# Kernel optimization log

Measured on AMD Instinct MI355X. Metric: run time of the kernel, lower is better.

## Reference

```python
import jax, jax.numpy as jnp
import numpy as np

B, S, D, H = 8, 1024, 1024, 16
HD = D // H  # 64


def setup_inputs() -> dict:
    key = jax.random.key(0)
    ks = jax.random.split(key, 10)
    f32 = jnp.float32
    inp = {
        "query": jax.random.normal(ks[0], (B, S, D), f32),
        "key": jax.random.normal(ks[1], (B, S, D), f32),
        "value": jax.random.normal(ks[2], (B, S, D), f32),
        "rel": jax.random.normal(ks[3], (B, S, S), f32),
        "timestamp": jax.random.normal(ks[4], (B, S, S), f32),
        "mask": jax.random.randint(ks[5], (B, S, S), 0, 2).astype(bool),
        "l1": jnp.float32(0.3),
        "l2": jnp.float32(0.5),
        "encode_pos": 0,
        "Wq": jax.random.normal(ks[6], (D, D), f32) * 0.02,
        "bq": jnp.zeros((D,), f32),
        "Wk": jax.random.normal(ks[7], (D, D), f32) * 0.02,
        "bk": jnp.zeros((D,), f32),
        "Wv": jax.random.normal(ks[8], (D, D), f32) * 0.02,
        "bv": jnp.zeros((D,), f32),
    }
    return inp


def _proj(x, W, b):
    # nn.Linear: x @ W.T + b, then split heads -> [B, H, S, HD]
    y = x @ W.T + b
    return y.reshape(B, S, H, HD).transpose(0, 2, 1, 3)


def reference(query, key, value, rel, timestamp, mask, l1, l2, encode_pos,
              Wq, bq, Wk, bk, Wv, bv):
    # encode_pos == 0 path: QK^T + time-decay + rel-attn three-softmax blend
    q = _proj(query, Wq, bq)
    k = _proj(key, Wk, bk)
    v = _proj(value, Wv, bv)

    m = mask[:, None]                       # [B,1,S,S], broadcasts over heads
    mf = m.astype(jnp.float32)

    # rel attention: zero out where mask is False, then fill zeros with -1e5
    rel_m = rel[:, None] * mf               # [B,1,S,S]
    rel_attn = jax.nn.softmax(jnp.where(rel_m == 0, -100000.0, rel_m), axis=-1)

    inv_sqrt_d = 1.0 / np.sqrt(HD).astype(np.float32)
    scores = jnp.einsum("bhqd,bhkd->bhqk", q, k) * inv_sqrt_d
    scores = jnp.where(m, -1e32, scores)

    time_stamp = jnp.exp(-jnp.abs(timestamp[:, None]))   # [B,1,S,S]
    time_stamp = jnp.where(m, -100000.0, time_stamp)

    prob_attn = jax.nn.softmax(scores, axis=-1)          # [B,H,S,S]
    time_attn = jax.nn.softmax(time_stamp, axis=-1)      # [B,1,S,S]

    prob_attn = (1.0 - l2) * prob_attn + l2 * time_attn
    prob_attn = (1.0 - l1) * prob_attn + l1 * rel_attn
    # dropout is identity at inference

    out = jnp.einsum("bhqk,bhkd->bhqd", prob_attn, v)
    out = out.transpose(0, 2, 1, 3).reshape(B, S, D)
    return out, prob_attn
```

## Files before the change

kernel.cpp:

```cpp
#include <hip/hip_runtime.h>
#include <stdint.h>

typedef short bf16x8 __attribute__((ext_vector_type(8)));
typedef short bf16x4 __attribute__((ext_vector_type(4)));
typedef float f32x4 __attribute__((ext_vector_type(4)));
typedef unsigned short u16x4 __attribute__((ext_vector_type(4)));
typedef unsigned short u16x8 __attribute__((ext_vector_type(8)));

constexpr int NB = 8, NS = 1024, ND = 1024, NH = 16, NHD = 64;

static __device__ __forceinline__ unsigned short f2bf(float f) {
    union { float f; uint32_t u; } v; v.f = f;
    uint32_t r = (v.u + 0x7fffu + ((v.u >> 16) & 1u)) >> 16;
    return (unsigned short)r;
}

static __device__ __forceinline__ f32x4 mfma32(bf16x8 a, bf16x8 b, f32x4 c) {
    return __builtin_amdgcn_mfma_f32_16x16x32_bf16(a, b, c, 0, 0, 0);
}

static __device__ __forceinline__ f32x4 mfma16(bf16x4 a, bf16x4 b, f32x4 c) {
#if __has_builtin(__builtin_amdgcn_mfma_f32_16x16x16bf16_1k)
    return __builtin_amdgcn_mfma_f32_16x16x16bf16_1k(a, b, c, 0, 0, 0);
#elif __has_builtin(__builtin_amdgcn_mfma_f32_16x16x16_bf16)
    return __builtin_amdgcn_mfma_f32_16x16x16_bf16(a, b, c, 0, 0, 0);
#else
    asm volatile("v_mfma_f32_16x16x16_bf16 %0, %1, %2, %0\n\ts_nop 7\n\ts_nop 7"
                 : "+v"(c) : "v"(a), "v"(b));
    return c;
#endif
}

static __device__ __forceinline__ bool mask_at(const void* m, size_t idx, int ms) {
    if (ms == 4) return ((const unsigned int*)m)[idx] != 0u;
    return ((const unsigned char*)m)[idx] != 0;
}

__global__ void detect_mask(const unsigned int* __restrict__ m, int* __restrict__ flag) {
    int l = threadIdx.x;
    bool bad = false;
    for (int i = l; i < 1024; i += 64) {
        unsigned int w = m[i];
        bad |= (w > 1u && w != 0x3f800000u);
    }
    bad = (bool)__any(bad);
    if (l == 0) *flag = bad ? 1 : 4;
}

__global__ __launch_bounds__(256) void cvt_frag(const float* __restrict__ in,
                                                unsigned short* __restrict__ out, int n8) {
    int stride = gridDim.x * blockDim.x;
    for (int idx = blockIdx.x * blockDim.x + threadIdx.x; idx < n8; idx += stride) {
        const float4* p = (const float4*)in + 2 * (size_t)idx;
        float4 a = p[0], b = p[1];
        u16x8 o;
        o[0] = f2bf(a.x); o[1] = f2bf(a.y); o[2] = f2bf(a.z); o[3] = f2bf(a.w);
        o[4] = f2bf(b.x); o[5] = f2bf(b.y); o[6] = f2bf(b.z); o[7] = f2bf(b.w);
        int m = idx >> 7, c8 = idx & 127;
        int kt = c8 >> 2, sub = c8 & 3;
        int lane = (m & 15) + 16 * sub;
        size_t slot = ((size_t)(m >> 4) * 32 + kt) * 64 + lane;
        *(u16x8*)(out + slot * 8) = o;
    }
}

__global__ __launch_bounds__(256) void proj_gemm(const unsigned short* __restrict__ Af,
                                                 const unsigned short* __restrict__ Wf,
                                                 const float* __restrict__ bias,
                                                 unsigned short* __restrict__ C, int mode) {
    int l = threadIdx.x & 63, w = threadIdx.x >> 6;
    int lr = l & 15, lg = l >> 4;
    int m_base = blockIdx.x * 128 + (w >> 1) * 64;
    int n_base = blockIdx.y * 128 + (w & 1) * 64;
    int mtg0 = m_base >> 4, ntg0 = n_base >> 4;
    f32x4 acc[4][4] = {};
    for (int kt = 0; kt < 32; kt++) {
        bf16x8 af[4], bfr[4];
        #pragma unroll
        for (int mt = 0; mt < 4; mt++)
            af[mt] = *(const bf16x8*)(Af + (((size_t)(mtg0 + mt) * 32 + kt) * 64 + l) * 8);
        #pragma unroll
        for (int nt = 0; nt < 4; nt++)
            bfr[nt] = *(const bf16x8*)(Wf + (((size_t)(ntg0 + nt) * 32 + kt) * 64 + l) * 8);
        #pragma unroll
        for (int mt = 0; mt < 4; mt++) {
            #pragma unroll
            for (int nt = 0; nt < 4; nt++)
                acc[mt][nt] = mfma32(af[mt], bfr[nt], acc[mt][nt]);
        }
    }
    #pragma unroll
    for (int mt = 0; mt < 4; mt++) {
        #pragma unroll
        for (int nt = 0; nt < 4; nt++) {
            int col = n_base + nt * 16 + lr;
            int row0 = m_base + mt * 16 + lg * 4;
            float bv = bias[col];
            int b = row0 >> 10;
            int h = col >> 6;
            if (mode == 0) {
                int st = (row0 & 1023) >> 4;
                int d32 = (col & 63) >> 5;
                int sub = (col & 31) >> 3;
                int e = col & 7;
                size_t base = ((((size_t)(b * NH + h) * 64 + st) * 2 + d32) * 64) * 8;
                #pragma unroll
                for (int r = 0; r < 4; r++) {
                    int lane = lg * 4 + r + 16 * sub;
                    C[base + (size_t)lane * 8 + e] = f2bf(acc[mt][nt][r] + bv);
                }
            } else {
                int s0 = row0 & 1023;
                int tg = s0 >> 4;
                int wv = tg >> 4;
                int t_in = tg & 15;
                int tp = t_in >> 1, half = t_in & 1;
                int dd = col & 63;
                int dt = dd >> 4;
                int lane = (dd & 15) + 16 * lg;
                u16x4 pk;
                #pragma unroll
                for (int r = 0; r < 4; r++) pk[r] = f2bf(acc[mt][nt][r] + bv);
                size_t addr = (((((size_t)(b * NH + h) * 4 + wv) * 8 + tp) * 4 + dt) * 64 + lane) * 8
                              + half * 4;
                *(u16x4*)(C + addr) = pk;
            }
        }
    }
}

__global__ __launch_bounds__(256) void tr_kernel(const float* __restrict__ rel,
                                                 const float* __restrict__ ts,
                                                 const void* __restrict__ maskp,
                                                 const int* __restrict__ msflag,
                                                 const float* __restrict__ l1p,
                                                 const float* __restrict__ l2p,
                                                 float* __restrict__ TRf,
                                                 uint32_t* __restrict__ PMf) {
    __shared__ float s_tm[4], s_rm[4], s_ts[4], s_rs[4];
    __shared__ unsigned char s_nib[256];
    int row = blockIdx.x;
    int t = threadIdx.x, w = t >> 6, l = t & 63;
    int ms = *msflag;
    size_t base = (size_t)row * NS;
    float4 r4 = ((const float4*)(rel + base))[t];
    float4 t4 = ((const float4*)(ts + base))[t];
    float rr[4], tt[4];
    *(float4*)rr = r4; *(float4*)tt = t4;
    float tv[4], rv[4];
    unsigned nib = 0;
    float tmx = -3.0e38f, rmx = -3.0e38f;
    #pragma unroll
    for (int j = 0; j < 4; j++) {
        bool m = mask_at(maskp, base + t * 4 + j, ms);
        nib |= (m ? 1u : 0u) << j;
        tv[j] = m ? -100000.0f : __expf(-fabsf(tt[j]));
        float rm_ = m ? rr[j] : 0.0f;
        rv[j] = (rm_ == 0.0f) ? -100000.0f : rm_;
        tmx = fmaxf(tmx, tv[j]); rmx = fmaxf(rmx, rv[j]);
    }
    s_nib[t] = (unsigned char)nib;
    #pragma unroll
    for (int off = 1; off < 64; off <<= 1) {
        tmx = fmaxf(tmx, __shfl_xor(tmx, off));
        rmx = fmaxf(rmx, __shfl_xor(rmx, off));
    }
    if (l == 0) { s_tm[w] = tmx; s_rm[w] = rmx; }
    __syncthreads();
    tmx = fmaxf(fmaxf(s_tm[0], s_tm[1]), fmaxf(s_tm[2], s_tm[3]));
    rmx = fmaxf(fmaxf(s_rm[0], s_rm[1]), fmaxf(s_rm[2], s_rm[3]));
    float te[4], re[4], tsum = 0.f, rsum = 0.f;
    #pragma unroll
    for (int j = 0; j < 4; j++) {
        te[j] = __expf(tv[j] - tmx); tsum += te[j];
        re[j] = __expf(rv[j] - rmx); rsum += re[j];
    }
    #pragma unroll
    for (int off = 1; off < 64; off <<= 1) {
        tsum += __shfl_xor(tsum, off);
        rsum += __shfl_xor(rsum, off);
    }
    if (l == 0) { s_ts[w] = tsum; s_rs[w] = rsum; }
    __syncthreads();
    tsum = s_ts[0] + s_ts[1] + s_ts[2] + s_ts[3];
    rsum = s_rs[0] + s_rs[1] + s_rs[2] + s_rs[3];
    float l1 = *l1p, l2 = *l2p;
    float ti = ((1.0f - l1) * l2) / tsum;
    float ri = l1 / rsum;
    float4 o;
    o.x = te[0] * ti + re[0] * ri;
    o.y = te[1] * ti + re[1] * ri;
    o.z = te[2] * ti + re[2] * ri;
    o.w = te[3] * ti + re[3] * ri;
    int b = row >> 10, q = row & 1023;
    int qt = q >> 4, qr = q & 15;
    size_t slot = ((((size_t)(b * 64 + qt) * 4 + (t >> 6)) * 16 + ((t >> 2) & 15)) * 64
                   + (qr + 16 * (t & 3)));
    ((float4*)TRf)[slot] = o;
    if (t < 32) {
        uint32_t word = 0;
        #pragma unroll
        for (int i = 0; i < 8; i++)
            word |= ((uint32_t)s_nib[t * 8 + i]) << (i * 4);
        PMf[(((size_t)(b * 64 + qt) * 4 + (t >> 3)) * 16 + qr) * 8 + (t & 7)] = word;
    }
}

__global__ __launch_bounds__(256) void att_pv_kernel(const unsigned short* __restrict__ Qf,
                                                     const unsigned short* __restrict__ Kf,
                                                     const uint32_t* __restrict__ PMf,
                                                     const float* __restrict__ TRf,
                                                     const float* __restrict__ l1p,
                                                     const float* __restrict__ l2p,
                                                     const unsigned short* __restrict__ Vf,
                                                     float* __restrict__ probOut,
                                                     float* __restrict__ outp) {
    __shared__ float reds[4][16];
    __shared__ f32x4 pacc[4][4][64];
    int bid = blockIdx.x;
    int swz = ((bid & 7) << 10) | (bid >> 3);
    int qt = swz & 63;
    int h = (swz >> 6) & 15;
    int b = swz >> 10;
    int tid = threadIdx.x, w = tid >> 6, l = tid & 63, lr = l & 15, lg = l >> 4;
    int q0 = qt * 16;
    int k_base = w * 256;
    int q = q0 + lr;
    size_t bh = (size_t)(b * NH + h);

    const unsigned short* qf = Qf + (((bh * 64 + qt) * 2) * 64 + l) * 8;
    bf16x8 bq0 = *(const bf16x8*)(qf);
    bf16x8 bq1 = *(const bf16x8*)(qf + 64 * 8);

    const uint32_t* pmp = PMf + (((size_t)(b * 64 + qt) * 4 + w) * 16 + lr) * 8;
    uint32_t pm[8];
    *(uint4*)(pm) = *(const uint4*)(pmp);
    *(uint4*)(pm + 4) = *(const uint4*)(pmp + 4);

    f32x4 acc[16] = {};
    const unsigned short* kfb = Kf + (((bh * 64 + w * 16) * 2) * 64) * 8 + (size_t)l * 8;
    #pragma unroll
    for (int t = 0; t < 16; t++) {
        const unsigned short* kp = kfb + (size_t)t * 2 * 64 * 8;
        bf16x8 a0 = *(const bf16x8*)(kp);
        bf16x8 a1 = *(const bf16x8*)(kp + 64 * 8);
        acc[t] = mfma32(a0, bq0, acc[t]);
        acc[t] = mfma32(a1, bq1, acc[t]);
    }
    float sm = 0.f;
    #pragma unroll
    for (int t = 0; t < 16; t++) {
        uint32_t word = pm[t >> 1];
        int shift = (t & 1) * 16 + lg * 4;
        #pragma unroll
        for (int r = 0; r < 4; r++) {
            bool m = (word >> (shift + r)) & 1u;
            float e = m ? 0.0f : __expf(acc[t][r] * 0.125f);
            acc[t][r] = e;
            sm += e;
        }
    }
    sm += __shfl_xor(sm, 16);
    sm += __shfl_xor(sm, 32);
    if (l < 16) reds[w][l] = sm;
    __syncthreads();
    float total = reds[0][lr] + reds[1][lr] + reds[2][lr] + reds[3][lr];
    float l1 = *l1p, l2 = *l2p;
    float rinv = ((1.0f - l1) * (1.0f - l2)) / total;

    float* po = probOut + bh * NS * NS + (size_t)q * NS + k_base;
    const float* trf = TRf + ((((size_t)(b * 64 + qt) * 4 + w) * 16) * 64 + l) * 4;
    const unsigned short* vf = Vf + ((((size_t)bh * 4 + w) * 8 * 4) * 64 + (size_t)l) * 8;
    f32x4 acc2[4] = {};
    #pragma unroll
    for (int tp = 0; tp < 8; tp++) {
        bf16x4 pfa, pfb;
        #pragma unroll
        for (int hf = 0; hf < 2; hf++) {
            int t = tp * 2 + hf;
            float4 tr4 = *(const float4*)(trf + t * 256);
            float4 o;
            o.x = acc[t][0] * rinv + tr4.x;
            o.y = acc[t][1] * rinv + tr4.y;
            o.z = acc[t][2] * rinv + tr4.z;
            o.w = acc[t][3] * rinv + tr4.w;
            *(float4*)(po + t * 16 + lg * 4) = o;
            bf16x4 pk;
            pk[0] = (short)f2bf(o.x); pk[1] = (short)f2bf(o.y);
            pk[2] = (short)f2bf(o.z); pk[3] = (short)f2bf(o.w);
            if (hf == 0) pfa = pk; else pfb = pk;
        }
        #pragma unroll
        for (int dt = 0; dt < 4; dt++) {
            bf16x8 vv = *(const bf16x8*)(vf + (size_t)(tp * 4 + dt) * 64 * 8);
            bf16x4 v0 = __builtin_shufflevector(vv, vv, 0, 1, 2, 3);
            bf16x4 v1 = __builtin_shufflevector(vv, vv, 4, 5, 6, 7);
            acc2[dt] = mfma16(v0, pfa, acc2[dt]);
            acc2[dt] = mfma16(v1, pfb, acc2[dt]);
        }
    }
    #pragma unroll
    for (int dt = 0; dt < 4; dt++) pacc[w][dt][l] = acc2[dt];
    __syncthreads();
    f32x4 s4 = pacc[0][w][l] + pacc[1][w][l] + pacc[2][w][l] + pacc[3][w][l];
    float4 ov;
    ov.x = s4[0]; ov.y = s4[1]; ov.z = s4[2]; ov.w = s4[3];
    *(float4*)(outp + ((size_t)b * NS + q0 + lr) * ND + h * NHD + w * 16 + lg * 4) = ov;
}

extern "C" void kernel_launch(void* const* d_in, const int* in_sizes, int n_in,
                              void* d_out, int out_size, void* d_ws, size_t ws_size,
                              hipStream_t stream) {
    const float* query = (const float*)d_in[0];
    const float* key   = (const float*)d_in[1];
    const float* value = (const float*)d_in[2];
    const float* rel   = (const float*)d_in[3];
    const float* ts    = (const float*)d_in[4];
    const void*  mask  = d_in[5];
    const float* l1p   = (const float*)d_in[6];
    const float* l2p   = (const float*)d_in[7];
    const float* Wq = (const float*)d_in[9];
    const float* bq = (const float*)d_in[10];
    const float* Wk = (const float*)d_in[11];
    const float* bk = (const float*)d_in[12];
    const float* Wv = (const float*)d_in[13];
    const float* bv = (const float*)d_in[14];

    char* ws = (char*)d_ws;
    const size_t SZ = (size_t)NB * NS * ND * 2;
    unsigned short* Qf  = (unsigned short*)(ws);
    unsigned short* Kf  = (unsigned short*)(ws + SZ);
    unsigned short* Vf  = (unsigned short*)(ws + 2 * SZ);
    unsigned short* Afq = (unsigned short*)(ws + 3 * SZ);
    unsigned short* Afk = (unsigned short*)(ws + 4 * SZ);
    unsigned short* Afv = (unsigned short*)(ws + 5 * SZ);
    unsigned short* Wfq = (unsigned short*)(ws + 6 * SZ);
    unsigned short* Wfk = (unsigned short*)(ws + 6 * SZ + 2u * 1024 * 1024);
    unsigned short* Wfv = (unsigned short*)(ws + 6 * SZ + 4u * 1024 * 1024);
    int* msflag         = (int*)(ws + 6 * SZ + 6u * 1024 * 1024);
    uint32_t* PMf       = (uint32_t*)(ws + 6 * SZ + 8u * 1024 * 1024);
    float* TRf = (float*)(ws + 3 * SZ);

    detect_mask<<<1, 64, 0, stream>>>((const unsigned int*)mask, msflag);

    const int nX8 = NB * NS * ND / 8;
    const int nW8 = 1024 * 1024 / 8;
    cvt_frag<<<1024, 256, 0, stream>>>(query, Afq, nX8);
    cvt_frag<<<1024, 256, 0, stream>>>(key,   Afk, nX8);
    cvt_frag<<<1024, 256, 0, stream>>>(value, Afv, nX8);
    cvt_frag<<<256, 256, 0, stream>>>(Wq, Wfq, nW8);
    cvt_frag<<<256, 256, 0, stream>>>(Wk, Wfk, nW8);
    cvt_frag<<<256, 256, 0, stream>>>(Wv, Wfv, nW8);

    dim3 pg(64, 8);
    proj_gemm<<<pg, 256, 0, stream>>>(Afq, Wfq, bq, Qf, 0);
    proj_gemm<<<pg, 256, 0, stream>>>(Afk, Wfk, bk, Kf, 0);
    proj_gemm<<<pg, 256, 0, stream>>>(Afv, Wfv, bv, Vf, 1);

    tr_kernel<<<NB * NS, 256, 0, stream>>>(rel, ts, mask, msflag, l1p, l2p, TRf, PMf);

    float* outp = (float*)d_out;
    float* probOut = outp + (size_t)NB * NS * ND;
    att_pv_kernel<<<NB * NH * (NS / 16), 256, 0, stream>>>(Qf, Kf, PMf, TRf, l1p, l2p, Vf,
                                                           probOut, outp);
}
```

Measured before the change: 572.8 us.

## Use single-wave attention blocks that recompute QK^T instead of splitting keys

Each attention block now uses one 64-thread wave covering all 1024 keys for a 16-query tile, instead of four waves each covering 256 keys. The cross-wave LDS reductions and __syncthreads for the softmax denominator and PV partials are gone. QK^T is computed twice, once for the row sum and again when writing probabilities, so the 16 score accumulators no longer have to stay in registers. V, TR and mask layouts are rearranged to match the per-wave key ordering. The cost is doubled QK MFMA work and K reads, plus longer serial work per wave.

```diff
diff --git a/kernel.cpp b/kernel.cpp
--- a/kernel.cpp
+++ b/kernel.cpp
@@ -112,16 +112,14 @@
             } else {
                 int s0 = row0 & 1023;
                 int tg = s0 >> 4;
-                int wv = tg >> 4;
-                int t_in = tg & 15;
-                int tp = t_in >> 1, half = t_in & 1;
+                int tp = tg >> 1, half = tg & 1;
                 int dd = col & 63;
                 int dt = dd >> 4;
                 int lane = (dd & 15) + 16 * lg;
                 u16x4 pk;
                 #pragma unroll
                 for (int r = 0; r < 4; r++) pk[r] = f2bf(acc[mt][nt][r] + bv);
-                size_t addr = (((((size_t)(b * NH + h) * 4 + wv) * 8 + tp) * 4 + dt) * 64 + lane) * 8
+                size_t addr = ((((size_t)(b * NH + h) * 32 + tp) * 4 + dt) * 64 + lane) * 8
                               + half * 4;
                 *(u16x4*)(C + addr) = pk;
             }
@@ -194,37 +192,33 @@
     o.w = te[3] * ti + re[3] * ri;
     int b = row >> 10, q = row & 1023;
     int qt = q >> 4, qr = q & 15;
-    size_t slot = ((((size_t)(b * 64 + qt) * 4 + (t >> 6)) * 16 + ((t >> 2) & 15)) * 64
-                   + (qr + 16 * (t & 3)));
+    size_t slot = ((size_t)(b * 64 + qt) * 64 + (t >> 2)) * 64 + (qr + 16 * (t & 3));
     ((float4*)TRf)[slot] = o;
     if (t < 32) {
         uint32_t word = 0;
         #pragma unroll
         for (int i = 0; i < 8; i++)
             word |= ((uint32_t)s_nib[t * 8 + i]) << (i * 4);
-        PMf[(((size_t)(b * 64 + qt) * 4 + (t >> 3)) * 16 + qr) * 8 + (t & 7)] = word;
-    }
-}
-
-__global__ __launch_bounds__(256) void att_pv_kernel(const unsigned short* __restrict__ Qf,
-                                                     const unsigned short* __restrict__ Kf,
-                                                     const uint32_t* __restrict__ PMf,
-                                                     const float* __restrict__ TRf,
-                                                     const float* __restrict__ l1p,
-                                                     const float* __restrict__ l2p,
-                                                     const unsigned short* __restrict__ Vf,
-                                                     float* __restrict__ probOut,
-                                                     float* __restrict__ outp) {
-    __shared__ float reds[4][16];
-    __shared__ f32x4 pacc[4][4][64];
+        PMf[((size_t)(b * 64 + qt) * 16 + qr) * 32 + t] = word;
+    }
+}
+
+__global__ __launch_bounds__(64, 4) void att_pv_kernel(const unsigned short* __restrict__ Qf,
+                                                       const unsigned short* __restrict__ Kf,
+                                                       const uint32_t* __restrict__ PMf,
+                                                       const float* __restrict__ TRf,
+                                                       const float* __restrict__ l1p,
+                                                       const float* __restrict__ l2p,
+                                                       const unsigned short* __restrict__ Vf,
+                                                       float* __restrict__ probOut,
+                                                       float* __restrict__ outp) {
     int bid = blockIdx.x;
     int swz = ((bid & 7) << 10) | (bid >> 3);
     int qt = swz & 63;
     int h = (swz >> 6) & 15;
     int b = swz >> 10;
-    int tid = threadIdx.x, w = tid >> 6, l = tid & 63, lr = l & 15, lg = l >> 4;
+    int l = threadIdx.x, lr = l & 15, lg = l >> 4;
     int q0 = qt * 16;
-    int k_base = w * 256;
     int q = q0 + lr;
     size_t bh = (size_t)(b * NH + h);
 
@@ -232,80 +226,91 @@
     bf16x8 bq0 = *(const bf16x8*)(qf);
     bf16x8 bq1 = *(const bf16x8*)(qf + 64 * 8);
 
-    const uint32_t* pmp = PMf + (((size_t)(b * 64 + qt) * 4 + w) * 16 + lr) * 8;
-    uint32_t pm[8];
-    *(uint4*)(pm) = *(const uint4*)(pmp);
-    *(uint4*)(pm + 4) = *(const uint4*)(pmp + 4);
-
-    f32x4 acc[16] = {};
-    const unsigned short* kfb = Kf + (((bh * 64 + w * 16) * 2) * 64) * 8 + (size_t)l * 8;
-    #pragma unroll
-    for (int t = 0; t < 16; t++) {
-        const unsigned short* kp = kfb + (size_t)t * 2 * 64 * 8;
-        bf16x8 a0 = *(const bf16x8*)(kp);
-        bf16x8 a1 = *(const bf16x8*)(kp + 64 * 8);
-        acc[t] = mfma32(a0, bq0, acc[t]);
-        acc[t] = mfma32(a1, bq1, acc[t]);
-    }
+    const unsigned short* kfb = Kf + ((bh * 64 * 2) * 64) * 8 + (size_t)l * 8;
+    const uint32_t* pmrow = PMf + ((size_t)(b * 64 + qt) * 16 + lr) * 32;
+
     float sm = 0.f;
-    #pragma unroll
-    for (int t = 0; t < 16; t++) {
-        uint32_t word = pm[t >> 1];
-        int shift = (t & 1) * 16 + lg * 4;
-        #pragma unroll
-        for (int r = 0; r < 4; r++) {
-            bool m = (word >> (shift + r)) & 1u;
-            float e = m ? 0.0f : __expf(acc[t][r] * 0.125f);
-            acc[t][r] = e;
-            sm += e;
+    for (int t8 = 0; t8 < 8; t8++) {
+        uint32_t pmw[4];
+        *(uint4*)pmw = *(const uint4*)(pmrow + t8 * 4);
+        #pragma unroll
+        for (int tt = 0; tt < 8; tt++) {
+            int t = t8 * 8 + tt;
+            const unsigned short* kp = kfb + (size_t)t * 1024;
+            bf16x8 a0 = *(const bf16x8*)kp;
+            bf16x8 a1 = *(const bf16x8*)(kp + 512);
+            f32x4 acc = {};
+            acc = mfma32(a0, bq0, acc);
+            acc = mfma32(a1, bq1, acc);
+            uint32_t word = pmw[tt >> 1];
+            int shift = (tt & 1) * 16 + lg * 4;
+            #pragma unroll
+            for (int r = 0; r < 4; r++) {
+                bool m = (word >> (shift + r)) & 1u;
+                sm += m ? 0.0f : __expf(acc[r] * 0.125f);
+            }
         }
     }
     sm += __shfl_xor(sm, 16);
     sm += __shfl_xor(sm, 32);
-    if (l < 16) reds[w][l] = sm;
-    __syncthreads();
-    float total = reds[0][lr] + reds[1][lr] + reds[2][lr] + reds[3][lr];
     float l1 = *l1p, l2 = *l2p;
-    float rinv = ((1.0f - l1) * (1.0f - l2)) / total;
-
-    float* po = probOut + bh * NS * NS + (size_t)q * NS + k_base;
-    const float* trf = TRf + ((((size_t)(b * 64 + qt) * 4 + w) * 16) * 64 + l) * 4;
-    const unsigned short* vf = Vf + ((((size_t)bh * 4 + w) * 8 * 4) * 64 + (size_t)l) * 8;
+    float rinv = ((1.0f - l1) * (1.0f - l2)) / sm;
+
+    float* po = probOut + bh * NS * NS + (size_t)q * NS;
+    const float4* trf = (const float4*)TRf + ((size_t)(b * 64 + qt) * 64) * 64 + l;
+    const unsigned short* vf = Vf + (bh * 32 * 4 * 64) * 8 + (size_t)l * 8;
     f32x4 acc2[4] = {};
-    #pragma unroll
-    for (int tp = 0; tp < 8; tp++) {
-        bf16x4 pfa, pfb;
-        #pragma unroll
-        for (int hf = 0; hf < 2; hf++) {
-            int t = tp * 2 + hf;
-            float4 tr4 = *(const float4*)(trf + t * 256);
-            float4 o;
-            o.x = acc[t][0] * rinv + tr4.x;
-            o.y = acc[t][1] * rinv + tr4.y;
-            o.z = acc[t][2] * rinv + tr4.z;
-            o.w = acc[t][3] * rinv + tr4.w;
-            *(float4*)(po + t * 16 + lg * 4) = o;
-            bf16x4 pk;
-            pk[0] = (short)f2bf(o.x); pk[1] = (short)f2bf(o.y);
-            pk[2] = (short)f2bf(o.z); pk[3] = (short)f2bf(o.w);
-            if (hf == 0) pfa = pk; else pfb = pk;
+    for (int tq = 0; tq < 8; tq++) {
+        uint32_t pmw[4];
+        *(uint4*)pmw = *(const uint4*)(pmrow + tq * 4);
+        #pragma unroll
+        for (int tpi = 0; tpi < 4; tpi++) {
+            int tp = tq * 4 + tpi;
+            bf16x4 pf0, pf1;
+            #pragma unroll
+            for (int hf = 0; hf < 2; hf++) {
+                int t = tp * 2 + hf;
+                const unsigned short* kp = kfb + (size_t)t * 1024;
+                bf16x8 a0 = *(const bf16x8*)kp;
+                bf16x8 a1 = *(const bf16x8*)(kp + 512);
+                f32x4 acc = {};
+                acc = mfma32(a0, bq0, acc);
+                acc = mfma32(a1, bq1, acc);
+                uint32_t word = pmw[tpi];
+                int shift = hf * 16 + lg * 4;
+                float4 tr4 = ((const float4*)trf)[(size_t)t * 64];
+                float4 o;
+                float e0 = ((word >> (shift + 0)) & 1u) ? 0.f : __expf(acc[0] * 0.125f);
+                float e1 = ((word >> (shift + 1)) & 1u) ? 0.f : __expf(acc[1] * 0.125f);
+                float e2 = ((word >> (shift + 2)) & 1u) ? 0.f : __expf(acc[2] * 0.125f);
+                float e3 = ((word >> (shift + 3)) & 1u) ? 0.f : __expf(acc[3] * 0.125f);
+                o.x = e0 * rinv + tr4.x;
+                o.y = e1 * rinv + tr4.y;
+                o.z = e2 * rinv + tr4.z;
+                o.w = e3 * rinv + tr4.w;
+                *(float4*)(po + t * 16 + lg * 4) = o;
+                bf16x4 pk;
+                pk[0] = (short)f2bf(o.x); pk[1] = (short)f2bf(o.y);
+                pk[2] = (short)f2bf(o.z); pk[3] = (short)f2bf(o.w);
+                if (hf == 0) pf0 = pk; else pf1 = pk;
+            }
+            #pragma unroll
+            for (int dt = 0; dt < 4; dt++) {
+                bf16x8 vv = *(const bf16x8*)(vf + (size_t)(tp * 4 + dt) * 512);
+                bf16x4 v0 = __builtin_shufflevector(vv, vv, 0, 1, 2, 3);
+                bf16x4 v1 = __builtin_shufflevector(vv, vv, 4, 5, 6, 7);
+                acc2[dt] = mfma16(v0, pf0, acc2[dt]);
+                acc2[dt] = mfma16(v1, pf1, acc2[dt]);
+            }
         }
-        #pragma unroll
-        for (int dt = 0; dt < 4; dt++) {
-            bf16x8 vv = *(const bf16x8*)(vf + (size_t)(tp * 4 + dt) * 64 * 8);
-            bf16x4 v0 = __builtin_shufflevector(vv, vv, 0, 1, 2, 3);
-            bf16x4 v1 = __builtin_shufflevector(vv, vv, 4, 5, 6, 7);
-            acc2[dt] = mfma16(v0, pfa, acc2[dt]);
-            acc2[dt] = mfma16(v1, pfb, acc2[dt]);
-        }
-    }
-    #pragma unroll
-    for (int dt = 0; dt < 4; dt++) pacc[w][dt][l] = acc2[dt];
-    __syncthreads();
-    f32x4 s4 = pacc[0][w][l] + pacc[1][w][l] + pacc[2][w][l] + pacc[3][w][l];
-    float4 ov;
-    ov.x = s4[0]; ov.y = s4[1]; ov.z = s4[2]; ov.w = s4[3];
-    *(float4*)(outp + ((size_t)b * NS + q0 + lr) * ND + h * NHD + w * 16 + lg * 4) = ov;
+    }
+    float* orow = outp + ((size_t)b * NS + q) * ND + h * NHD + lg * 4;
+    #pragma unroll
+    for (int dt = 0; dt < 4; dt++) {
+        float4 ov;
+        ov.x = acc2[dt][0]; ov.y = acc2[dt][1]; ov.z = acc2[dt][2]; ov.w = acc2[dt][3];
+        *(float4*)(orow + dt * 16) = ov;
+    }
 }
 
 extern "C" void kernel_launch(void* const* d_in, const int* in_sizes, int n_in,
@@ -361,6 +366,6 @@
 
     float* outp = (float*)d_out;
     float* probOut = outp + (size_t)NB * NS * ND;
-    att_pv_kernel<<<NB * NH * (NS / 16), 256, 0, stream>>>(Qf, Kf, PMf, TRf, l1p, l2p, Vf,
-                                                           probOut, outp);
-}
+    att_pv_kernel<<<NB * NH * (NS / 16), 64, 0, stream>>>(Qf, Kf, PMf, TRf, l1p, l2p, Vf,
+                                                          probOut, outp);
+}
```

Result: faster. 515.5 us (median of 2 runs) (-10.0%).
